# Optimization experiments

Measured on AMD Instinct MI355X. Metric: run time of the kernel, lower is better.

## Reference

```python
import jax, jax.numpy as jnp
import numpy as np

NUM_NODES = 50000


def setup_inputs() -> dict:
    key = jax.random.key(0)
    ks = jax.random.split(key, 5)
    d = 128
    E = 600000
    x = jax.random.normal(ks[0], (NUM_NODES, d), dtype=jnp.float32)
    edge_attr = jax.random.normal(ks[1], (E, d), dtype=jnp.float32)
    receivers_idx = jax.random.randint(ks[2], (E,), 0, NUM_NODES)
    # MLP params: Linear(2d -> d), ReLU, Linear(d -> d). Stored as [in, out].
    W1 = jax.random.normal(ks[3], (2 * d, d), dtype=jnp.float32) / np.sqrt(2 * d)
    b1 = jnp.zeros((d,), dtype=jnp.float32)
    W2 = jax.random.normal(ks[4], (d, d), dtype=jnp.float32) / np.sqrt(d)
    b2 = jnp.zeros((d,), dtype=jnp.float32)
    return {"x": x, "edge_attr": edge_attr, "receivers_idx": receivers_idx,
            "W1": W1, "b1": b1, "W2": W2, "b2": b2}


def reference(x, edge_attr, receivers_idx, W1, b1, W2, b2):
    # scatter_add(edge_attr, receivers_idx, dim=0, dim_size=num_nodes)
    agg = jax.ops.segment_sum(edge_attr, receivers_idx, num_segments=NUM_NODES)  # [N, d]
    collected = jnp.concatenate([x, agg], axis=-1)  # [N, 2d]
    h = jax.nn.relu(collected @ W1 + b1)  # [N, d]
    out = h @ W2 + b2                     # [N, d]
    # Original returns Data(x=out, edge_attr=edge_attr, edge_index=edge_index);
    # edge_attr/edge_index pass through unchanged, so return the new node features.
    return out
```

## Files before the change

### kernel.cpp

```cpp
#include <hip/hip_runtime.h>
#include <hip/hip_bf16.h>

#define N_NODES 50000
#define DIM 128
#define N_EDGES 600000
#define MAX_DEG 64

typedef __attribute__((ext_vector_type(8))) short short8;
typedef __attribute__((ext_vector_type(4))) float f32x4;

__device__ __forceinline__ unsigned short f2bf_u(float f) {
    return __bfloat16_as_ushort(__float2bfloat16(f));
}

#define FILL_BLOCKS ((N_EDGES + 255) / 256)
#define PREP_BLOCKS 192

__global__ __launch_bounds__(256) void fill_prep(
    const int* __restrict__ ridx, int* __restrict__ cnt, int* __restrict__ elist,
    const float* __restrict__ W1, const float* __restrict__ W2,
    __hip_bfloat16* __restrict__ W1t, __hip_bfloat16* __restrict__ W2t) {
    int b = blockIdx.x;
    if (b < FILL_BLOCKS) {
        int e = b * 256 + threadIdx.x;
        if (e < N_EDGES) {
            int node = ridx[e];
            int pos = atomicAdd(&cnt[node], 1);
            if (pos < MAX_DEG) elist[(size_t)node * MAX_DEG + pos] = e;
        }
    } else {
        int t = (b - FILL_BLOCKS) * 256 + threadIdx.x;
        if (t < 256 * 128) {
            int k = t >> 7, n = t & 127;
            W1t[n * 256 + k] = __float2bfloat16(W1[t]);
        } else {
            int q = t - 256 * 128;
            int k = q >> 7, n = q & 127;
            W2t[n * 128 + k] = __float2bfloat16(W2[q]);
        }
    }
}

__global__ __launch_bounds__(512) void gather_mlp(
    const float* __restrict__ x,
    const float* __restrict__ edge_attr,
    const int* __restrict__ elist,
    const int* __restrict__ cnt,
    const __hip_bfloat16* __restrict__ W1t,
    const float* __restrict__ b1,
    const __hip_bfloat16* __restrict__ W2t,
    const float* __restrict__ b2,
    float* __restrict__ out) {
    __shared__ __hip_bfloat16 sIn[32][264];
    __shared__ __hip_bfloat16 sH[32][136];

    const int wave = threadIdx.x >> 6;
    const int lane = threadIdx.x & 63;
    const int quad = lane >> 4;
    const int l16  = lane & 15;
    const int rowBase = blockIdx.x * 32;

    for (int i = 0; i < 4; i++) {
        const int r = wave * 4 + i;
        const int node = rowBase + r;
        unsigned px = 0u, pa = 0u;
        if (node < N_NODES) {
            float2 xv = *reinterpret_cast<const float2*>(x + (size_t)node * DIM + lane * 2);
            px = ((unsigned)f2bf_u(xv.y) << 16) | (unsigned)f2bf_u(xv.x);
            int deg = cnt[node];
            deg = deg < MAX_DEG ? deg : MAX_DEG;
            const int* el = elist + (size_t)node * MAX_DEG;
            float sx = 0.f, sy = 0.f;
            int j = 0;
            for (; j + 8 <= deg; j += 8) {
                int4 ea = *reinterpret_cast<const int4*>(el + j);
                int4 eb = *reinterpret_cast<const int4*>(el + j + 4);
                float2 v0 = *reinterpret_cast<const float2*>(edge_attr + (size_t)ea.x * DIM + lane * 2);
                float2 v1 = *reinterpret_cast<const float2*>(edge_attr + (size_t)ea.y * DIM + lane * 2);
                float2 v2 = *reinterpret_cast<const float2*>(edge_attr + (size_t)ea.z * DIM + lane * 2);
                float2 v3 = *reinterpret_cast<const float2*>(edge_attr + (size_t)ea.w * DIM + lane * 2);
                float2 v4 = *reinterpret_cast<const float2*>(edge_attr + (size_t)eb.x * DIM + lane * 2);
                float2 v5 = *reinterpret_cast<const float2*>(edge_attr + (size_t)eb.y * DIM + lane * 2);
                float2 v6 = *reinterpret_cast<const float2*>(edge_attr + (size_t)eb.z * DIM + lane * 2);
                float2 v7 = *reinterpret_cast<const float2*>(edge_attr + (size_t)eb.w * DIM + lane * 2);
                sx += ((v0.x + v1.x) + (v2.x + v3.x)) + ((v4.x + v5.x) + (v6.x + v7.x));
                sy += ((v0.y + v1.y) + (v2.y + v3.y)) + ((v4.y + v5.y) + (v6.y + v7.y));
            }
            if (j + 4 <= deg) {
                int4 ea = *reinterpret_cast<const int4*>(el + j);
                float2 v0 = *reinterpret_cast<const float2*>(edge_attr + (size_t)ea.x * DIM + lane * 2);
                float2 v1 = *reinterpret_cast<const float2*>(edge_attr + (size_t)ea.y * DIM + lane * 2);
                float2 v2 = *reinterpret_cast<const float2*>(edge_attr + (size_t)ea.z * DIM + lane * 2);
                float2 v3 = *reinterpret_cast<const float2*>(edge_attr + (size_t)ea.w * DIM + lane * 2);
                sx += (v0.x + v1.x) + (v2.x + v3.x);
                sy += (v0.y + v1.y) + (v2.y + v3.y);
                j += 4;
            }
            for (; j < deg; j++) {
                int e0 = el[j];
                float2 v0 = *reinterpret_cast<const float2*>(edge_attr + (size_t)e0 * DIM + lane * 2);
                sx += v0.x;
                sy += v0.y;
            }
            pa = ((unsigned)f2bf_u(sy) << 16) | (unsigned)f2bf_u(sx);
        }
        *reinterpret_cast<unsigned*>(&sIn[r][lane * 2]) = px;
        *reinterpret_cast<unsigned*>(&sIn[r][128 + lane * 2]) = pa;
    }
    __syncthreads();

    const int wm = wave >> 2;
    const int colBase = (wave & 3) * 32;

    f32x4 accH[2] = {};
#pragma unroll
    for (int ks = 0; ks < 8; ks++) {
        const int k0 = ks * 32 + quad * 8;
        short8 a = *reinterpret_cast<const short8*>(&sIn[wm * 16 + l16][k0]);
#pragma unroll
        for (int nt = 0; nt < 2; nt++) {
            short8 b = *reinterpret_cast<const short8*>(W1t + (colBase + nt * 16 + l16) * 256 + k0);
            accH[nt] = __builtin_amdgcn_mfma_f32_16x16x32_bf16(a, b, accH[nt], 0, 0, 0);
        }
    }

#pragma unroll
    for (int nt = 0; nt < 2; nt++) {
        const float bias = b1[colBase + nt * 16 + l16];
#pragma unroll
        for (int i = 0; i < 4; i++) {
            float v = accH[nt][i] + bias;
            v = v > 0.0f ? v : 0.0f;
            sH[wm * 16 + quad * 4 + i][colBase + nt * 16 + l16] = __float2bfloat16(v);
        }
    }
    __syncthreads();

    f32x4 accO[2] = {};
#pragma unroll
    for (int ks = 0; ks < 4; ks++) {
        const int k0 = ks * 32 + quad * 8;
        short8 a = *reinterpret_cast<const short8*>(&sH[wm * 16 + l16][k0]);
#pragma unroll
        for (int nt = 0; nt < 2; nt++) {
            short8 b = *reinterpret_cast<const short8*>(W2t + (colBase + nt * 16 + l16) * 128 + k0);
            accO[nt] = __builtin_amdgcn_mfma_f32_16x16x32_bf16(a, b, accO[nt], 0, 0, 0);
        }
    }

#pragma unroll
    for (int nt = 0; nt < 2; nt++) {
        const float bias = b2[colBase + nt * 16 + l16];
#pragma unroll
        for (int i = 0; i < 4; i++) {
            int row = rowBase + wm * 16 + quad * 4 + i;
            if (row < N_NODES) {
                out[(size_t)row * DIM + colBase + nt * 16 + l16] = accO[nt][i] + bias;
            }
        }
    }
}

extern "C" void kernel_launch(void* const* d_in, const int* in_sizes, int n_in,
                              void* d_out, int out_size, void* d_ws, size_t ws_size,
                              hipStream_t stream) {
    const float* x         = (const float*)d_in[0];
    const float* edge_attr = (const float*)d_in[1];
    const int*   ridx      = (const int*)d_in[2];
    const float* W1        = (const float*)d_in[3];
    const float* b1        = (const float*)d_in[4];
    const float* W2        = (const float*)d_in[5];
    const float* b2        = (const float*)d_in[6];
    float* out = (float*)d_out;

    char* w = (char*)d_ws;
    int* elist = (int*)w;                     w += (size_t)N_NODES * MAX_DEG * 4;
    int* cnt   = (int*)w;                     w += (size_t)N_NODES * 4;
    __hip_bfloat16* W1t = (__hip_bfloat16*)w; w += 256 * 128 * 2;
    __hip_bfloat16* W2t = (__hip_bfloat16*)w;

    hipMemsetAsync(cnt, 0, (size_t)N_NODES * 4, stream);
    fill_prep<<<dim3(FILL_BLOCKS + PREP_BLOCKS), dim3(256), 0, stream>>>(
        ridx, cnt, elist, W1, W2, W1t, W2t);
    gather_mlp<<<dim3((N_NODES + 31) / 32), dim3(512), 0, stream>>>(
        x, edge_attr, elist, cnt, W1t, b1, W2t, b2, out);
}
```

Baseline: 519.3 us.

## Gather two nodes per wave with float4 loads and predicated fixed-depth edge unroll

Each wave now handles two nodes at once, with half-waves loading float4 (16B) edge_attr chunks instead of float2. The first 16 edge slots are issued unconditionally, with masked indices and predicated adds, so many independent gathers are in flight at once. Only the tail past 16 edges uses a loop. The intent is higher memory-level parallelism and fewer serialized per-node loops. The cost is extra loads of edge 0 for padded slots and reading uninitialized elist entries, which stay masked.

```diff
diff --git a/kernel.cpp b/kernel.cpp
--- a/kernel.cpp
+++ b/kernel.cpp
@@ -11,6 +11,24 @@
 
 __device__ __forceinline__ unsigned short f2bf_u(float f) {
     return __bfloat16_as_ushort(__float2bfloat16(f));
+}
+
+__device__ __forceinline__ uint2 pack4(f32x4 v) {
+    ushort2 a = { f2bf_u(v[0]), f2bf_u(v[1]) };
+    ushort2 b = { f2bf_u(v[2]), f2bf_u(v[3]) };
+    uint2 r = { *reinterpret_cast<unsigned*>(&a), *reinterpret_cast<unsigned*>(&b) };
+    return r;
+}
+
+__device__ __forceinline__ void acc_edge(f32x4& s, const float* __restrict__ ea,
+                                         int e, int k, int deg, int d0) {
+    const int es = k < deg ? e : 0;
+    f32x4 v = *reinterpret_cast<const f32x4*>(ea + (size_t)es * DIM + d0);
+    const bool p = k < deg;
+    s[0] += p ? v[0] : 0.f;
+    s[1] += p ? v[1] : 0.f;
+    s[2] += p ? v[2] : 0.f;
+    s[3] += p ? v[3] : 0.f;
 }
 
 #define FILL_BLOCKS ((N_EDGES + 255) / 256)
@@ -60,52 +78,61 @@
     const int l16  = lane & 15;
     const int rowBase = blockIdx.x * 32;
 
-    for (int i = 0; i < 4; i++) {
-        const int r = wave * 4 + i;
-        const int node = rowBase + r;
-        unsigned px = 0u, pa = 0u;
-        if (node < N_NODES) {
-            float2 xv = *reinterpret_cast<const float2*>(x + (size_t)node * DIM + lane * 2);
-            px = ((unsigned)f2bf_u(xv.y) << 16) | (unsigned)f2bf_u(xv.x);
-            int deg = cnt[node];
-            deg = deg < MAX_DEG ? deg : MAX_DEG;
-            const int* el = elist + (size_t)node * MAX_DEG;
-            float sx = 0.f, sy = 0.f;
-            int j = 0;
-            for (; j + 8 <= deg; j += 8) {
-                int4 ea = *reinterpret_cast<const int4*>(el + j);
-                int4 eb = *reinterpret_cast<const int4*>(el + j + 4);
-                float2 v0 = *reinterpret_cast<const float2*>(edge_attr + (size_t)ea.x * DIM + lane * 2);
-                float2 v1 = *reinterpret_cast<const float2*>(edge_attr + (size_t)ea.y * DIM + lane * 2);
-                float2 v2 = *reinterpret_cast<const float2*>(edge_attr + (size_t)ea.z * DIM + lane * 2);
-                float2 v3 = *reinterpret_cast<const float2*>(edge_attr + (size_t)ea.w * DIM + lane * 2);
-                float2 v4 = *reinterpret_cast<const float2*>(edge_attr + (size_t)eb.x * DIM + lane * 2);
-                float2 v5 = *reinterpret_cast<const float2*>(edge_attr + (size_t)eb.y * DIM + lane * 2);
-                float2 v6 = *reinterpret_cast<const float2*>(edge_attr + (size_t)eb.z * DIM + lane * 2);
-                float2 v7 = *reinterpret_cast<const float2*>(edge_attr + (size_t)eb.w * DIM + lane * 2);
-                sx += ((v0.x + v1.x) + (v2.x + v3.x)) + ((v4.x + v5.x) + (v6.x + v7.x));
-                sy += ((v0.y + v1.y) + (v2.y + v3.y)) + ((v4.y + v5.y) + (v6.y + v7.y));
-            }
-            if (j + 4 <= deg) {
-                int4 ea = *reinterpret_cast<const int4*>(el + j);
-                float2 v0 = *reinterpret_cast<const float2*>(edge_attr + (size_t)ea.x * DIM + lane * 2);
-                float2 v1 = *reinterpret_cast<const float2*>(edge_attr + (size_t)ea.y * DIM + lane * 2);
-                float2 v2 = *reinterpret_cast<const float2*>(edge_attr + (size_t)ea.z * DIM + lane * 2);
-                float2 v3 = *reinterpret_cast<const float2*>(edge_attr + (size_t)ea.w * DIM + lane * 2);
-                sx += (v0.x + v1.x) + (v2.x + v3.x);
-                sy += (v0.y + v1.y) + (v2.y + v3.y);
-                j += 4;
-            }
-            for (; j < deg; j++) {
-                int e0 = el[j];
-                float2 v0 = *reinterpret_cast<const float2*>(edge_attr + (size_t)e0 * DIM + lane * 2);
-                sx += v0.x;
-                sy += v0.y;
-            }
-            pa = ((unsigned)f2bf_u(sy) << 16) | (unsigned)f2bf_u(sx);
-        }
-        *reinterpret_cast<unsigned*>(&sIn[r][lane * 2]) = px;
-        *reinterpret_cast<unsigned*>(&sIn[r][128 + lane * 2]) = pa;
+    {
+        const int h   = lane >> 5;
+        const int l32 = lane & 31;
+        const int d0  = l32 * 4;
+
+        const int r0 = wave * 4 + h;
+        const int r1 = r0 + 2;
+        const int n0 = rowBase + r0;
+        const int n1 = rowBase + r1;
+        const int nc0 = n0 < N_NODES ? n0 : N_NODES - 1;
+        const int nc1 = n1 < N_NODES ? n1 : N_NODES - 1;
+
+        f32x4 xv0 = *reinterpret_cast<const f32x4*>(x + (size_t)nc0 * DIM + d0);
+        f32x4 xv1 = *reinterpret_cast<const f32x4*>(x + (size_t)nc1 * DIM + d0);
+
+        int deg0 = cnt[nc0];
+        int deg1 = cnt[nc1];
+        deg0 = n0 < N_NODES ? (deg0 < MAX_DEG ? deg0 : MAX_DEG) : 0;
+        deg1 = n1 < N_NODES ? (deg1 < MAX_DEG ? deg1 : MAX_DEG) : 0;
+
+        const int* el0 = elist + (size_t)nc0 * MAX_DEG;
+        const int* el1 = elist + (size_t)nc1 * MAX_DEG;
+
+        int4 q0[4], q1[4];
+#pragma unroll
+        for (int c = 0; c < 4; c++) {
+            q0[c] = *reinterpret_cast<const int4*>(el0 + c * 4);
+            q1[c] = *reinterpret_cast<const int4*>(el1 + c * 4);
+        }
+
+        f32x4 s0 = {}, s1 = {};
+#pragma unroll
+        for (int c = 0; c < 4; c++) {
+            acc_edge(s0, edge_attr, q0[c].x, c * 4 + 0, deg0, d0);
+            acc_edge(s1, edge_attr, q1[c].x, c * 4 + 0, deg1, d0);
+            acc_edge(s0, edge_attr, q0[c].y, c * 4 + 1, deg0, d0);
+            acc_edge(s1, edge_attr, q1[c].y, c * 4 + 1, deg1, d0);
+            acc_edge(s0, edge_attr, q0[c].z, c * 4 + 2, deg0, d0);
+            acc_edge(s1, edge_attr, q1[c].z, c * 4 + 2, deg1, d0);
+            acc_edge(s0, edge_attr, q0[c].w, c * 4 + 3, deg0, d0);
+            acc_edge(s1, edge_attr, q1[c].w, c * 4 + 3, deg1, d0);
+        }
+        for (int j = 16; j < deg0; j++) {
+            f32x4 v = *reinterpret_cast<const f32x4*>(edge_attr + (size_t)el0[j] * DIM + d0);
+            s0[0] += v[0]; s0[1] += v[1]; s0[2] += v[2]; s0[3] += v[3];
+        }
+        for (int j = 16; j < deg1; j++) {
+            f32x4 v = *reinterpret_cast<const f32x4*>(edge_attr + (size_t)el1[j] * DIM + d0);
+            s1[0] += v[0]; s1[1] += v[1]; s1[2] += v[2]; s1[3] += v[3];
+        }
+
+        *reinterpret_cast<uint2*>(&sIn[r0][d0])       = pack4(xv0);
+        *reinterpret_cast<uint2*>(&sIn[r0][128 + d0]) = pack4(s0);
+        *reinterpret_cast<uint2*>(&sIn[r1][d0])       = pack4(xv1);
+        *reinterpret_cast<uint2*>(&sIn[r1][128 + d0]) = pack4(s1);
     }
     __syncthreads();
 
```

Result: no change. 514.2 us (-1.0%).
